# Optimization experiments

Hardware: AMD Instinct MI355X
Metric: run time of the kernel (lower is better)

Reference implementation:

```python
import jax, jax.numpy as jnp
import numpy as np
import math

D_MODEL = 1024
NUM_HEADS = 16
D_K = D_MODEL // NUM_HEADS
B, S = 2, 2048


def setup_inputs() -> dict:
    key = jax.random.key(0)
    ks = jax.random.split(key, 13)
    scale = 1.0 / math.sqrt(D_MODEL)
    inp = {
        "q": jax.random.normal(ks[0], (B, S, D_MODEL), jnp.float32),
        "k": jax.random.normal(ks[1], (B, S, D_MODEL), jnp.float32),
        "v": jax.random.normal(ks[2], (B, S, D_MODEL), jnp.float32),
        "mask": jax.random.randint(ks[3], (B, 1, S, S), 0, 2, jnp.int32),
        # torch nn.Linear params: y = x @ W.T + b
        "wQ_w": jax.random.normal(ks[4], (D_MODEL, D_MODEL), jnp.float32) * scale,
        "wQ_b": jax.random.normal(ks[5], (D_MODEL,), jnp.float32) * scale,
        "wK_w": jax.random.normal(ks[6], (D_MODEL, D_MODEL), jnp.float32) * scale,
        "wK_b": jax.random.normal(ks[7], (D_MODEL,), jnp.float32) * scale,
        "wV_w": jax.random.normal(ks[8], (D_MODEL, D_MODEL), jnp.float32) * scale,
        "wV_b": jax.random.normal(ks[9], (D_MODEL,), jnp.float32) * scale,
        "wO_w": jax.random.normal(ks[10], (D_MODEL, D_MODEL), jnp.float32) * scale,
        "wO_b": jax.random.normal(ks[11], (D_MODEL,), jnp.float32) * scale,
    }
    return inp


def _split_heads(x):
    # [B, S, D] -> [B, H, S, dK]
    b, s, _ = x.shape
    return x.reshape(b, s, NUM_HEADS, D_K).transpose(0, 2, 1, 3)


def reference(q, k, v, mask, wQ_w, wQ_b, wK_w, wK_b, wV_w, wV_b, wO_w, wO_b):
    qh = _split_heads(q @ wQ_w.T + wQ_b)
    kh = _split_heads(k @ wK_w.T + wK_b)
    vh = _split_heads(v @ wV_w.T + wV_b)
    # scores: [B, H, S, S] -- materialized as in the original module
    scores = jnp.einsum("bhsd,bhtd->bhst", qh, kh) / math.sqrt(D_K)
    scores = jnp.where(mask == 0, jnp.float32(-1e9), scores)
    attn = jax.nn.softmax(scores, axis=-1)
    out = jnp.einsum("bhst,bhtd->bhsd", attn, vh)  # [B, H, S, dK]
    out = out.transpose(0, 2, 1, 3).reshape(q.shape[0], -1, D_MODEL)
    return out @ wO_w.T + wO_b
```

## Files before the change

kernel.cpp:

```cpp
#include <hip/hip_runtime.h>
#include <hip/hip_bf16.h>
#include <stdint.h>
#include <math.h>

#define NHEADS 16
#define DK 64
#define BATCH 2
#define SEQ 2048
#define DMODEL 1024
#define MROWS (BATCH*SEQ)

typedef __bf16 bf16x8 __attribute__((ext_vector_type(8)));
typedef float  f32x4  __attribute__((ext_vector_type(4)));
typedef float  f32x16 __attribute__((ext_vector_type(16)));

typedef const __attribute__((address_space(1))) void* gas_ptr;
typedef       __attribute__((address_space(3))) void* las_ptr;

__device__ __forceinline__ void async16(const void* g, void* l) {
  __builtin_amdgcn_global_load_lds((gas_ptr)g, (las_ptr)l, 16, 0, 0);
}

__device__ __forceinline__ unsigned short f2bf_raw(float f) {
  __hip_bfloat16 h = __float2bfloat16(f);
  return *reinterpret_cast<unsigned short*>(&h);
}

__device__ __forceinline__ float fast_exp2(float x) {
#if __has_builtin(__builtin_amdgcn_exp2f)
  return __builtin_amdgcn_exp2f(x);
#else
  float r;
  asm("v_exp_f32 %0, %1\ns_nop 1" : "=v"(r) : "v"(x));
  return r;
#endif
}

__device__ __forceinline__ uint32_t pk_bf16(float lo, float hi2) {
  uint32_t r;
  asm("v_cvt_pk_bf16_f32 %0, %1, %2" : "=v"(r) : "v"(lo), "v"(hi2));
  return r;
}

__device__ __forceinline__ void half_swap(uint32_t& a, uint32_t& b) {
  auto r = __builtin_amdgcn_permlane32_swap(a, b, false, false);
  a = (uint32_t)r[0];
  b = (uint32_t)r[1];
}

__device__ __forceinline__ float mask_sel(uint32_t msel, float s, float c) {
  uint32_t su = __float_as_uint(s), cu = __float_as_uint(c);
  return __uint_as_float((msel & su) | (~msel & cu));
}

__device__ __forceinline__ f32x16 zero16() {
  f32x16 z;
#pragma unroll
  for (int i = 0; i < 16; ++i) z[i] = 0.f;
  return z;
}

__global__ void prep_kernel(const float* __restrict__ q,
                            const float* __restrict__ k,
                            const float* __restrict__ v,
                            const float* __restrict__ w0,
                            const float* __restrict__ w1,
                            const float* __restrict__ w2,
                            const float* __restrict__ w3,
                            ushort4* __restrict__ out,
                            const int* __restrict__ mask,
                            uint32_t* __restrict__ bits) {
  if (blockIdx.x < 16384) {
    int i = blockIdx.x * 256 + threadIdx.x;
    const float* src;
    int local;
    if (i < 3145728) {
      int seg = i >> 20;
      src = (seg == 0) ? q : (seg == 1) ? k : v;
      local = i & 1048575;
    } else {
      int j = i - 3145728;
      int seg = j >> 18;
      src = (seg == 0) ? w0 : (seg == 1) ? w1 : (seg == 2) ? w2 : w3;
      local = j & 262143;
    }
    float4 f = reinterpret_cast<const float4*>(src)[local];
    ushort4 u;
    u.x = f2bf_raw(f.x); u.y = f2bf_raw(f.y);
    u.z = f2bf_raw(f.z); u.w = f2bf_raw(f.w);
    out[i] = u;
  } else {
    int bi = blockIdx.x - 16384;
    int lane = threadIdx.x & 63, wid = threadIdx.x >> 6;
    size_t base = (size_t)bi * 1024 + (size_t)wid * 256;
    int4 q4 = reinterpret_cast<const int4*>(mask + base)[lane];
    uint32_t nib = (q4.x != 0 ? 1u : 0u) | (q4.y != 0 ? 2u : 0u) |
                   (q4.z != 0 ? 4u : 0u) | (q4.w != 0 ? 8u : 0u);
    nib <<= (lane & 7) * 4;
    nib |= (uint32_t)__shfl_xor((int)nib, 1);
    nib |= (uint32_t)__shfl_xor((int)nib, 2);
    nib |= (uint32_t)__shfl_xor((int)nib, 4);
    if ((lane & 7) == 0) bits[(base >> 5) + (lane >> 3)] = nib;
  }
}


__device__ __forceinline__ void gemm_core_128(
    const __hip_bfloat16* __restrict__ A, const __hip_bfloat16* __restrict__ Bw,
    int K, int m0, int n0,
    __hip_bfloat16* sA, __hip_bfloat16* sB, f32x4 acc[4][4]) {
  const int lane = threadIdx.x & 63;
  const int wid  = threadIdx.x >> 6;
  const int wr = wid >> 1, wc = wid & 1;
  const int l15 = lane & 15, lg = lane >> 4;
  const int sw = l15 & 7;
  const int crow8 = lane >> 3;
  const int cslot = lane & 7;

#pragma unroll
  for (int mi = 0; mi < 4; ++mi)
#pragma unroll
    for (int ni = 0; ni < 4; ++ni) acc[mi][ni] = f32x4{0.f, 0.f, 0.f, 0.f};

  for (int k0 = 0; k0 < K; k0 += 64) {
#pragma unroll
    for (int c0 = 0; c0 < 4; ++c0) {
      int c = wid + c0 * 4;
      int row = c * 8 + crow8;
      int scol = (cslot ^ (row & 7)) * 8;
      async16(A  + (size_t)(m0 + row) * K + k0 + scol,
              (char*)sA + c * 1024 + lane * 16);
      async16(Bw + (size_t)(n0 + row) * K + k0 + scol,
              (char*)sB + c * 1024 + lane * 16);
    }
    __syncthreads();
#pragma unroll
    for (int kc = 0; kc < 2; ++kc) {
      bf16x8 af[4], bfr[4];
#pragma unroll
      for (int mi = 0; mi < 4; ++mi)
        af[mi] = *reinterpret_cast<const bf16x8*>(
            &sA[(wr * 64 + mi * 16 + l15) * 64 + (((kc * 4 + lg) ^ sw) * 8)]);
#pragma unroll
      for (int ni = 0; ni < 4; ++ni)
        bfr[ni] = *reinterpret_cast<const bf16x8*>(
            &sB[(wc * 64 + ni * 16 + l15) * 64 + (((kc * 4 + lg) ^ sw) * 8)]);
      __builtin_amdgcn_s_setprio(1);
#pragma unroll
      for (int mi = 0; mi < 4; ++mi)
#pragma unroll
        for (int ni = 0; ni < 4; ++ni)
          acc[mi][ni] = __builtin_amdgcn_mfma_f32_16x16x32_bf16(
              af[mi], bfr[ni], acc[mi][ni], 0, 0, 0);
      __builtin_amdgcn_s_setprio(0);
    }
    __syncthreads();
  }
}

__global__ __launch_bounds__(256, 3) void qkv_gemm_kernel(
    const __hip_bfloat16* __restrict__ Xq, const __hip_bfloat16* __restrict__ Xk,
    const __hip_bfloat16* __restrict__ Xv,
    const __hip_bfloat16* __restrict__ Wq, const __hip_bfloat16* __restrict__ Wk,
    const __hip_bfloat16* __restrict__ Wv,
    const float* __restrict__ bq, const float* __restrict__ bk,
    const float* __restrict__ bv,
    __hip_bfloat16* __restrict__ Qh, __hip_bfloat16* __restrict__ Kh,
    __hip_bfloat16* __restrict__ VhT) {
  __shared__ __attribute__((aligned(16))) char smem[128 * 136 * 2];
  __hip_bfloat16* sA = (__hip_bfloat16*)smem;
  __hip_bfloat16* sB = (__hip_bfloat16*)(smem + 16384);
  const int z = blockIdx.z;
  const __hip_bfloat16* A  = (z == 0) ? Xq : (z == 1) ? Xk : Xv;
  const __hip_bfloat16* Bw = (z == 0) ? Wq : (z == 1) ? Wk : Wv;
  const float* bias        = (z == 0) ? bq : (z == 1) ? bk : bv;
  __hip_bfloat16* Co       = (z == 0) ? Qh : (z == 1) ? Kh : VhT;
  const int m0 = blockIdx.x * 128, n0 = blockIdx.y * 128;
  f32x4 acc[4][4];
  gemm_core_128(A, Bw, DMODEL, m0, n0, sA, sB, acc);

  const int tid = threadIdx.x, lane = tid & 63, wid = tid >> 6;
  const int wr = wid >> 1, wc = wid & 1;
  const int l15 = lane & 15, lg = lane >> 4;
  const float osc = (z == 0) ? 0.18033688f : 1.0f;
  const int PITCH = 136;
  __hip_bfloat16* sT = (__hip_bfloat16*)smem;

  if (z != 2) {
#pragma unroll
    for (int mi = 0; mi < 4; ++mi)
#pragma unroll
      for (int ni = 0; ni < 4; ++ni) {
        int jl = wc * 64 + ni * 16 + l15;
        float bj = bias[n0 + jl];
#pragma unroll
        for (int r = 0; r < 4; ++r) {
          int il = wr * 64 + mi * 16 + lg * 4 + r;
          sT[il * PITCH + jl] = __float2bfloat16((acc[mi][ni][r] + bj) * osc);
        }
      }
    __syncthreads();
#pragma unroll
    for (int u = 0; u < 8; ++u) {
      int t2 = tid + u * 256;
      int row = t2 >> 4, c8 = (t2 & 15) * 8;
      bf16x8 val = *reinterpret_cast<const bf16x8*>(&sT[row * PITCH + c8]);
      int ig = m0 + row, jg = n0 + c8;
      int bb = ig >> 11, s = ig & 2047, hh = jg >> 6, d = jg & 63;
      *reinterpret_cast<bf16x8*>(
          &Co[((size_t)(bb * NHEADS + hh) * SEQ + s) * DK + d]) = val;
    }
  } else {
#pragma unroll
    for (int mi = 0; mi < 4; ++mi)
#pragma unroll
      for (int ni = 0; ni < 4; ++ni) {
        int jl = wc * 64 + ni * 16 + l15;
        float bj = bias[n0 + jl];
        int il0 = wr * 64 + mi * 16 + lg * 4;
        ushort4 st4;
        st4.x = f2bf_raw(acc[mi][ni][0] + bj);
        st4.y = f2bf_raw(acc[mi][ni][1] + bj);
        st4.z = f2bf_raw(acc[mi][ni][2] + bj);
        st4.w = f2bf_raw(acc[mi][ni][3] + bj);
        *reinterpret_cast<ushort4*>(&sT[jl * PITCH + il0]) = st4;
      }
    __syncthreads();
#pragma unroll
    for (int u = 0; u < 8; ++u) {
      int t2 = tid + u * 256;
      int row = t2 >> 4, i8 = (t2 & 15) * 8;
      bf16x8 val = *reinterpret_cast<const bf16x8*>(&sT[row * PITCH + i8]);
      int jg = n0 + row, hh = jg >> 6, d = jg & 63;
      int ig0 = m0 + i8, bb = ig0 >> 11, s0 = ig0 & 2047;
      *reinterpret_cast<bf16x8*>(
          &Co[((size_t)(bb * NHEADS + hh) * DK + d) * SEQ + s0]) = val;
    }
  }
}

__global__ __launch_bounds__(256, 3) void out_gemm_kernel(
    const __hip_bfloat16* __restrict__ A, const __hip_bfloat16* __restrict__ Ww,
    const float* __restrict__ bias, float* __restrict__ C) {
  __shared__ __attribute__((aligned(16))) char smem[32768];
  __hip_bfloat16* sA = (__hip_bfloat16*)smem;
  __hip_bfloat16* sB = (__hip_bfloat16*)(smem + 16384);
  const int m0 = blockIdx.x * 128, n0 = blockIdx.y * 128;
  f32x4 acc[4][4];
  gemm_core_128(A, Ww, DMODEL, m0, n0, sA, sB, acc);
  const int lane = threadIdx.x & 63, wid = threadIdx.x >> 6;
  const int wr = wid >> 1, wc = wid & 1;
#pragma unroll
  for (int mi = 0; mi < 4; ++mi)
#pragma unroll
    for (int ni = 0; ni < 4; ++ni) {
      int j = n0 + wc * 64 + ni * 16 + (lane & 15);
      float bj = bias[j];
#pragma unroll
      for (int r = 0; r < 4; ++r) {
        int i = m0 + wr * 64 + mi * 16 + (lane >> 4) * 4 + r;
        C[(size_t)i * DMODEL + j] = acc[mi][ni][r] + bj;
      }
    }
}


__global__ __launch_bounds__(512, 4) void attn_kernel(
    const __hip_bfloat16* __restrict__ Qh, const __hip_bfloat16* __restrict__ Kh,
    const __hip_bfloat16* __restrict__ VhT, const uint32_t* __restrict__ mbits,
    __hip_bfloat16* __restrict__ AO) {
  __shared__ char pool[65536 + 512 + 512];
  __hip_bfloat16* Kpool = (__hip_bfloat16*)pool;
  __hip_bfloat16* Vpool = (__hip_bfloat16*)(pool + 32768);
  float* sRed = (float*)(pool + 65536);
  float* lC   = (float*)(pool + 65536 + 512);
  float* accC = (float*)pool;

  const int tid = threadIdx.x, lane = tid & 63, wid = tid >> 6;
  const int grp = wid >> 2, wq = wid & 3;
  const int ltid = tid & 255;
  const int l31 = lane & 31, hi = lane >> 5;
  const int sw = l31 & 7;
  const int bh = blockIdx.y, b = bh >> 4, h = bh & 15;
  const int q0g = blockIdx.x * 128 + wq * 32;
  const int kvbase = grp * (SEQ / 2);

  const __hip_bfloat16* Qp = Qh  + (size_t)bh * SEQ * DK;
  const __hip_bfloat16* Kp = Kh  + (size_t)bh * SEQ * DK;
  const __hip_bfloat16* Vp = VhT + (size_t)bh * DK * SEQ;
  const uint32_t* mb = mbits + (size_t)b * SEQ * (SEQ / 32)
                             + (size_t)(q0g + l31) * (SEQ / 32) + (kvbase >> 5);
  float* sRedW = &sRed[wq * 32];

  bf16x8 qf[4];
#pragma unroll
  for (int dc = 0; dc < 4; ++dc)
    qf[dc] = *reinterpret_cast<const bf16x8*>(
        &Qp[(size_t)(q0g + l31) * DK + dc * 16 + hi * 8]);

  f32x16 acc0 = zero16(), acc1 = zero16();
  float l_run = 0.f;

#define STAGE(kv0_, s_)                                                        \
  {                                                                            \
    _Pragma("unroll")                                                          \
    for (int u = 0; u < 2; ++u) {                                              \
      int c = ltid + u * 256;                                                  \
      int row = c >> 3, ss = (c & 7) ^ (row & 7);                              \
      async16(Kp + (size_t)(kvbase + (kv0_) + row) * DK + ss * 8,              \
              (char*)(Kpool + (grp * 2 + (s_)) * 4096) + c * 16);              \
      async16(Vp + (size_t)row * SEQ + kvbase + (kv0_) + ss * 8,               \
              (char*)(Vpool + (grp * 2 + (s_)) * 4096) + c * 16);              \
    }                                                                          \
  }

  STAGE(0, 0);
  uint2 mw = *reinterpret_cast<const uint2*>(mb);
  asm volatile("s_waitcnt vmcnt(0)" ::: "memory");
  __syncthreads();

  const int NT = SEQ / 2 / 64;
  for (int t = 0; t < NT; ++t) {
    const int cur = t & 1;
    if (t + 1 < NT) STAGE((t + 1) * 64, cur ^ 1);

    uint2 mw_next;
    if (t + 1 < NT) mw_next = *reinterpret_cast<const uint2*>(mb + (t + 1) * 2);
    uint32_t w0 = mw.x >> (4 * hi), w1 = mw.y >> (4 * hi);

    const __hip_bfloat16* ks = Kpool + (grp * 2 + cur) * 4096;
    const __hip_bfloat16* vs = Vpool + (grp * 2 + cur) * 4096;

    f32x16 s0 = zero16(), s1 = zero16();
    __builtin_amdgcn_s_setprio(1);
#pragma unroll
    for (int dc = 0; dc < 4; ++dc) {
      bf16x8 k0 = *reinterpret_cast<const bf16x8*>(
          &ks[(size_t)(l31) * 64 + (((dc * 2 + hi) ^ sw) * 8)]);
      bf16x8 k1 = *reinterpret_cast<const bf16x8*>(
          &ks[(size_t)(32 + l31) * 64 + (((dc * 2 + hi) ^ sw) * 8)]);
      s0 = __builtin_amdgcn_mfma_f32_32x32x16_bf16(k0, qf[dc], s0, 0, 0, 0);
      s1 = __builtin_amdgcn_mfma_f32_32x32x16_bf16(k1, qf[dc], s1, 0, 0, 0);
    }
    __builtin_amdgcn_s_setprio(0);

    union { uint32_t u[4]; bf16x8 v; } pc;
    {
      float p[16];
#pragma unroll
      for (int r = 0; r < 16; ++r) {
        const int sh = (r & 3) + 8 * (r >> 2);
        uint32_t msel = (uint32_t)__builtin_amdgcn_sbfe((int)w0, sh, 1);
        p[r] = fast_exp2(mask_sel(msel, s0[r], -1e9f));
        l_run += p[r];
      }
      uint32_t a0 = pk_bf16(p[0], p[1]),  a1 = pk_bf16(p[2], p[3]);
      uint32_t b0 = pk_bf16(p[4], p[5]),  b1 = pk_bf16(p[6], p[7]);
      uint32_t c0 = pk_bf16(p[8], p[9]),  c1 = pk_bf16(p[10], p[11]);
      uint32_t d0 = pk_bf16(p[12], p[13]), d1 = pk_bf16(p[14], p[15]);
      half_swap(a0, b0); half_swap(a1, b1);
      half_swap(c0, d0); half_swap(c1, d1);
      __builtin_amdgcn_s_setprio(1);
      pc.u[0] = a0; pc.u[1] = a1; pc.u[2] = b0; pc.u[3] = b1;
      {
        bf16x8 v0 = *reinterpret_cast<const bf16x8*>(
            &vs[(size_t)(l31) * 64 + (((0 + hi) ^ sw) * 8)]);
        bf16x8 v1 = *reinterpret_cast<const bf16x8*>(
            &vs[(size_t)(32 + l31) * 64 + (((0 + hi) ^ sw) * 8)]);
        acc0 = __builtin_amdgcn_mfma_f32_32x32x16_bf16(pc.v, v0, acc0, 0, 0, 0);
        acc1 = __builtin_amdgcn_mfma_f32_32x32x16_bf16(pc.v, v1, acc1, 0, 0, 0);
      }
      pc.u[0] = c0; pc.u[1] = c1; pc.u[2] = d0; pc.u[3] = d1;
      {
        bf16x8 v0 = *reinterpret_cast<const bf16x8*>(
            &vs[(size_t)(l31) * 64 + (((2 + hi) ^ sw) * 8)]);
        bf16x8 v1 = *reinterpret_cast<const bf16x8*>(
            &vs[(size_t)(32 + l31) * 64 + (((2 + hi) ^ sw) * 8)]);
        acc0 = __builtin_amdgcn_mfma_f32_32x32x16_bf16(pc.v, v0, acc0, 0, 0, 0);
        acc1 = __builtin_amdgcn_mfma_f32_32x32x16_bf16(pc.v, v1, acc1, 0, 0, 0);
      }
      __builtin_amdgcn_s_setprio(0);
    }
    {
      float p[16];
#pragma unroll
      for (int r = 0; r < 16; ++r) {
        const int sh = (r & 3) + 8 * (r >> 2);
        uint32_t msel = (uint32_t)__builtin_amdgcn_sbfe((int)w1, sh, 1);
        p[r] = fast_exp2(mask_sel(msel, s1[r], -1e9f));
        l_run += p[r];
      }
      uint32_t a0 = pk_bf16(p[0], p[1]),  a1 = pk_bf16(p[2], p[3]);
      uint32_t b0 = pk_bf16(p[4], p[5]),  b1 = pk_bf16(p[6], p[7]);
      uint32_t c0 = pk_bf16(p[8], p[9]),  c1 = pk_bf16(p[10], p[11]);
      uint32_t d0 = pk_bf16(p[12], p[13]), d1 = pk_bf16(p[14], p[15]);
      half_swap(a0, b0); half_swap(a1, b1);
      half_swap(c0, d0); half_swap(c1, d1);
      __builtin_amdgcn_s_setprio(1);
      pc.u[0] = a0; pc.u[1] = a1; pc.u[2] = b0; pc.u[3] = b1;
      {
        bf16x8 v0 = *reinterpret_cast<const bf16x8*>(
            &vs[(size_t)(l31) * 64 + (((4 + hi) ^ sw) * 8)]);
        bf16x8 v1 = *reinterpret_cast<const bf16x8*>(
            &vs[(size_t)(32 + l31) * 64 + (((4 + hi) ^ sw) * 8)]);
        acc0 = __builtin_amdgcn_mfma_f32_32x32x16_bf16(pc.v, v0, acc0, 0, 0, 0);
        acc1 = __builtin_amdgcn_mfma_f32_32x32x16_bf16(pc.v, v1, acc1, 0, 0, 0);
      }
      pc.u[0] = c0; pc.u[1] = c1; pc.u[2] = d0; pc.u[3] = d1;
      {
        bf16x8 v0 = *reinterpret_cast<const bf16x8*>(
            &vs[(size_t)(l31) * 64 + (((6 + hi) ^ sw) * 8)]);
        bf16x8 v1 = *reinterpret_cast<const bf16x8*>(
            &vs[(size_t)(32 + l31) * 64 + (((6 + hi) ^ sw) * 8)]);
        acc0 = __builtin_amdgcn_mfma_f32_32x32x16_bf16(pc.v, v0, acc0, 0, 0, 0);
        acc1 = __builtin_amdgcn_mfma_f32_32x32x16_bf16(pc.v, v1, acc1, 0, 0, 0);
      }
      __builtin_amdgcn_s_setprio(0);
    }

    mw = mw_next;
    asm volatile("s_waitcnt vmcnt(0)" ::: "memory");
    __syncthreads();
  }

  l_run += __shfl_xor(l_run, 32);

  if (grp == 1) {
    float* myacc = &accC[(wq * 64 + lane) * 32];
#pragma unroll
    for (int r = 0; r < 16; ++r) { myacc[r] = acc0[r]; myacc[16 + r] = acc1[r]; }
    if (hi == 0) lC[wq * 32 + l31] = l_run;
  }
  __syncthreads();

  if (grp == 0) {
    const float* oacc = &accC[(wq * 64 + lane) * 32];
#pragma unroll
    for (int r = 0; r < 16; ++r) { acc0[r] += oacc[r]; acc1[r] += oacc[16 + r]; }
    float l_tot = l_run + lC[wq * 32 + l31];
    if (hi == 0) sRedW[l31] = l_tot;
    asm volatile("s_waitcnt lgkmcnt(0)" ::: "memory");
#pragma unroll
    for (int r = 0; r < 16; ++r) {
      int cr = (r & 3) + 8 * (r >> 2) + 4 * hi;
      float linv = 1.0f / sRedW[cr];
      int qrow = q0g + cr;
      size_t base = ((size_t)b * SEQ + qrow) * DMODEL + h * 64 + l31;
      AO[base]      = __float2bfloat16(acc0[r] * linv);
      AO[base + 32] = __float2bfloat16(acc1[r] * linv);
    }
  }
}


extern "C" void kernel_launch(void* const* d_in, const int* in_sizes, int n_in,
                              void* d_out, int out_size, void* d_ws, size_t ws_size,
                              hipStream_t stream) {
  const float* q    = (const float*)d_in[0];
  const float* k    = (const float*)d_in[1];
  const float* v    = (const float*)d_in[2];
  const int*   mask = (const int*)d_in[3];
  const float* wQ_w = (const float*)d_in[4];
  const float* wQ_b = (const float*)d_in[5];
  const float* wK_w = (const float*)d_in[6];
  const float* wK_b = (const float*)d_in[7];
  const float* wV_w = (const float*)d_in[8];
  const float* wV_b = (const float*)d_in[9];
  const float* wO_w = (const float*)d_in[10];
  const float* wO_b = (const float*)d_in[11];

  char* ws = (char*)d_ws;
  const size_t SZ_X = (size_t)MROWS * DMODEL * 2;
  const size_t SZ_W = (size_t)DMODEL * DMODEL * 2;
  __hip_bfloat16* Xq  = (__hip_bfloat16*)(ws);
  __hip_bfloat16* Xk  = (__hip_bfloat16*)(ws + SZ_X);
  __hip_bfloat16* Xv  = (__hip_bfloat16*)(ws + 2 * SZ_X);
  __hip_bfloat16* Wq  = (__hip_bfloat16*)(ws + 3 * SZ_X);
  __hip_bfloat16* Wk  = (__hip_bfloat16*)(ws + 3 * SZ_X + SZ_W);
  __hip_bfloat16* Wv  = (__hip_bfloat16*)(ws + 3 * SZ_X + 2 * SZ_W);
  __hip_bfloat16* Wo  = (__hip_bfloat16*)(ws + 3 * SZ_X + 3 * SZ_W);
  __hip_bfloat16* Qh  = (__hip_bfloat16*)(ws + 3 * SZ_X + 4 * SZ_W);
  __hip_bfloat16* Kh  = (__hip_bfloat16*)(ws + 4 * SZ_X + 4 * SZ_W);
  __hip_bfloat16* VhT = (__hip_bfloat16*)(ws + 5 * SZ_X + 4 * SZ_W);
  __hip_bfloat16* AO  = (__hip_bfloat16*)(ws + 6 * SZ_X + 4 * SZ_W);
  uint32_t*       MB  = (uint32_t*)      (ws + 7 * SZ_X + 4 * SZ_W);

  prep_kernel<<<24576, 256, 0, stream>>>(q, k, v, wQ_w, wK_w, wV_w, wO_w,
                                         (ushort4*)ws, mask, MB);

  qkv_gemm_kernel<<<dim3(MROWS / 128, DMODEL / 128, 3), 256, 0, stream>>>(
      Xq, Xk, Xv, Wq, Wk, Wv, wQ_b, wK_b, wV_b, Qh, Kh, VhT);

  attn_kernel<<<dim3(SEQ / 128, BATCH * NHEADS), 512, 0, stream>>>(
      Qh, Kh, VhT, MB, AO);

  out_gemm_kernel<<<dim3(MROWS / 128, DMODEL / 128), 256, 0, stream>>>(
      AO, Wo, wO_b, (float*)d_out);
}
```

Baseline: 237.8 us.

## Split prep kernel, halve out-GEMM tile rows, launch attention per batch

Splits the combined cast/mask prep kernel into two separate kernels. Rewrites the output GEMM to use 64x128 tiles with a single-stage LDS load per k-step, which doubles the grid to fill more CUs. Splits the attention launch into two per-batch launches via a head offset. These changes aim to improve occupancy and load balance, at the cost of extra launch overhead and a GEMM loop that no longer overlaps loads with compute.

```diff
diff --git a/kernel.cpp b/kernel.cpp
--- a/kernel.cpp
+++ b/kernel.cpp
@@ -60,48 +60,47 @@
   return z;
 }
 
-__global__ void prep_kernel(const float* __restrict__ q,
+__global__ void cast_kernel(const float* __restrict__ q,
                             const float* __restrict__ k,
                             const float* __restrict__ v,
                             const float* __restrict__ w0,
                             const float* __restrict__ w1,
                             const float* __restrict__ w2,
                             const float* __restrict__ w3,
-                            ushort4* __restrict__ out,
-                            const int* __restrict__ mask,
+                            ushort4* __restrict__ out) {
+  int i = blockIdx.x * 256 + threadIdx.x;
+  const float* src;
+  int local;
+  if (i < 3145728) {
+    int seg = i >> 20;
+    src = (seg == 0) ? q : (seg == 1) ? k : v;
+    local = i & 1048575;
+  } else {
+    int j = i - 3145728;
+    int seg = j >> 18;
+    src = (seg == 0) ? w0 : (seg == 1) ? w1 : (seg == 2) ? w2 : w3;
+    local = j & 262143;
+  }
+  float4 f = reinterpret_cast<const float4*>(src)[local];
+  ushort4 u;
+  u.x = f2bf_raw(f.x); u.y = f2bf_raw(f.y);
+  u.z = f2bf_raw(f.z); u.w = f2bf_raw(f.w);
+  out[i] = u;
+}
+
+__global__ void mask_kernel(const int* __restrict__ mask,
                             uint32_t* __restrict__ bits) {
-  if (blockIdx.x < 16384) {
-    int i = blockIdx.x * 256 + threadIdx.x;
-    const float* src;
-    int local;
-    if (i < 3145728) {
-      int seg = i >> 20;
-      src = (seg == 0) ? q : (seg == 1) ? k : v;
-      local = i & 1048575;
-    } else {
-      int j = i - 3145728;
-      int seg = j >> 18;
-      src = (seg == 0) ? w0 : (seg == 1) ? w1 : (seg == 2) ? w2 : w3;
-      local = j & 262143;
-    }
-    float4 f = reinterpret_cast<const float4*>(src)[local];
-    ushort4 u;
-    u.x = f2bf_raw(f.x); u.y = f2bf_raw(f.y);
-    u.z = f2bf_raw(f.z); u.w = f2bf_raw(f.w);
-    out[i] = u;
-  } else {
-    int bi = blockIdx.x - 16384;
-    int lane = threadIdx.x & 63, wid = threadIdx.x >> 6;
-    size_t base = (size_t)bi * 1024 + (size_t)wid * 256;
-    int4 q4 = reinterpret_cast<const int4*>(mask + base)[lane];
-    uint32_t nib = (q4.x != 0 ? 1u : 0u) | (q4.y != 0 ? 2u : 0u) |
-                   (q4.z != 0 ? 4u : 0u) | (q4.w != 0 ? 8u : 0u);
-    nib <<= (lane & 7) * 4;
-    nib |= (uint32_t)__shfl_xor((int)nib, 1);
-    nib |= (uint32_t)__shfl_xor((int)nib, 2);
-    nib |= (uint32_t)__shfl_xor((int)nib, 4);
-    if ((lane & 7) == 0) bits[(base >> 5) + (lane >> 3)] = nib;
-  }
+  int bi = blockIdx.x;
+  int lane = threadIdx.x & 63, wid = threadIdx.x >> 6;
+  size_t base = (size_t)bi * 1024 + (size_t)wid * 256;
+  int4 q4 = reinterpret_cast<const int4*>(mask + base)[lane];
+  uint32_t nib = (q4.x != 0 ? 1u : 0u) | (q4.y != 0 ? 2u : 0u) |
+                 (q4.z != 0 ? 4u : 0u) | (q4.w != 0 ? 8u : 0u);
+  nib <<= (lane & 7) * 4;
+  nib |= (uint32_t)__shfl_xor((int)nib, 1);
+  nib |= (uint32_t)__shfl_xor((int)nib, 2);
+  nib |= (uint32_t)__shfl_xor((int)nib, 4);
+  if ((lane & 7) == 0) bits[(base >> 5) + (lane >> 3)] = nib;
 }
 
 
@@ -242,23 +241,73 @@
 __global__ __launch_bounds__(256, 3) void out_gemm_kernel(
     const __hip_bfloat16* __restrict__ A, const __hip_bfloat16* __restrict__ Ww,
     const float* __restrict__ bias, float* __restrict__ C) {
-  __shared__ __attribute__((aligned(16))) char smem[32768];
+  __shared__ __attribute__((aligned(16))) char smem[8192 + 16384];
   __hip_bfloat16* sA = (__hip_bfloat16*)smem;
-  __hip_bfloat16* sB = (__hip_bfloat16*)(smem + 16384);
-  const int m0 = blockIdx.x * 128, n0 = blockIdx.y * 128;
-  f32x4 acc[4][4];
-  gemm_core_128(A, Ww, DMODEL, m0, n0, sA, sB, acc);
+  __hip_bfloat16* sB = (__hip_bfloat16*)(smem + 8192);
+  const int m0 = blockIdx.x * 64, n0 = blockIdx.y * 128;
   const int lane = threadIdx.x & 63, wid = threadIdx.x >> 6;
   const int wr = wid >> 1, wc = wid & 1;
-#pragma unroll
-  for (int mi = 0; mi < 4; ++mi)
+  const int l15 = lane & 15, lg = lane >> 4;
+  const int sw = l15 & 7;
+  const int crow8 = lane >> 3;
+  const int cslot = lane & 7;
+
+  f32x4 acc[2][4];
+#pragma unroll
+  for (int mi = 0; mi < 2; ++mi)
+#pragma unroll
+    for (int ni = 0; ni < 4; ++ni) acc[mi][ni] = f32x4{0.f, 0.f, 0.f, 0.f};
+
+  for (int k0 = 0; k0 < DMODEL; k0 += 64) {
+#pragma unroll
+    for (int c0 = 0; c0 < 2; ++c0) {
+      int c = wid + c0 * 4;
+      int row = c * 8 + crow8;
+      int scol = (cslot ^ (row & 7)) * 8;
+      async16(A + (size_t)(m0 + row) * DMODEL + k0 + scol,
+              (char*)sA + c * 1024 + lane * 16);
+    }
+#pragma unroll
+    for (int c0 = 0; c0 < 4; ++c0) {
+      int c = wid + c0 * 4;
+      int row = c * 8 + crow8;
+      int scol = (cslot ^ (row & 7)) * 8;
+      async16(Ww + (size_t)(n0 + row) * DMODEL + k0 + scol,
+              (char*)sB + c * 1024 + lane * 16);
+    }
+    __syncthreads();
+#pragma unroll
+    for (int kc = 0; kc < 2; ++kc) {
+      bf16x8 af[2], bfr[4];
+#pragma unroll
+      for (int mi = 0; mi < 2; ++mi)
+        af[mi] = *reinterpret_cast<const bf16x8*>(
+            &sA[(wr * 32 + mi * 16 + l15) * 64 + (((kc * 4 + lg) ^ sw) * 8)]);
+#pragma unroll
+      for (int ni = 0; ni < 4; ++ni)
+        bfr[ni] = *reinterpret_cast<const bf16x8*>(
+            &sB[(wc * 64 + ni * 16 + l15) * 64 + (((kc * 4 + lg) ^ sw) * 8)]);
+      __builtin_amdgcn_s_setprio(1);
+#pragma unroll
+      for (int mi = 0; mi < 2; ++mi)
+#pragma unroll
+        for (int ni = 0; ni < 4; ++ni)
+          acc[mi][ni] = __builtin_amdgcn_mfma_f32_16x16x32_bf16(
+              af[mi], bfr[ni], acc[mi][ni], 0, 0, 0);
+      __builtin_amdgcn_s_setprio(0);
+    }
+    __syncthreads();
+  }
+
+#pragma unroll
+  for (int mi = 0; mi < 2; ++mi)
 #pragma unroll
     for (int ni = 0; ni < 4; ++ni) {
-      int j = n0 + wc * 64 + ni * 16 + (lane & 15);
+      int j = n0 + wc * 64 + ni * 16 + l15;
       float bj = bias[j];
 #pragma unroll
       for (int r = 0; r < 4; ++r) {
-        int i = m0 + wr * 64 + mi * 16 + (lane >> 4) * 4 + r;
+        int i = m0 + wr * 32 + mi * 16 + lg * 4 + r;
         C[(size_t)i * DMODEL + j] = acc[mi][ni][r] + bj;
       }
     }
@@ -268,7 +317,7 @@
 __global__ __launch_bounds__(512, 4) void attn_kernel(
     const __hip_bfloat16* __restrict__ Qh, const __hip_bfloat16* __restrict__ Kh,
     const __hip_bfloat16* __restrict__ VhT, const uint32_t* __restrict__ mbits,
-    __hip_bfloat16* __restrict__ AO) {
+    __hip_bfloat16* __restrict__ AO, int bh0) {
   __shared__ char pool[65536 + 512 + 512];
   __hip_bfloat16* Kpool = (__hip_bfloat16*)pool;
   __hip_bfloat16* Vpool = (__hip_bfloat16*)(pool + 32768);
@@ -281,7 +330,7 @@
   const int ltid = tid & 255;
   const int l31 = lane & 31, hi = lane >> 5;
   const int sw = l31 & 7;
-  const int bh = blockIdx.y, b = bh >> 4, h = bh & 15;
+  const int bh = bh0 + blockIdx.y, b = bh >> 4, h = bh & 15;
   const int q0g = blockIdx.x * 128 + wq * 32;
   const int kvbase = grp * (SEQ / 2);
 
@@ -485,15 +534,18 @@
   __hip_bfloat16* AO  = (__hip_bfloat16*)(ws + 6 * SZ_X + 4 * SZ_W);
   uint32_t*       MB  = (uint32_t*)      (ws + 7 * SZ_X + 4 * SZ_W);
 
-  prep_kernel<<<24576, 256, 0, stream>>>(q, k, v, wQ_w, wK_w, wV_w, wO_w,
-                                         (ushort4*)ws, mask, MB);
+  cast_kernel<<<16384, 256, 0, stream>>>(q, k, v, wQ_w, wK_w, wV_w, wO_w,
+                                         (ushort4*)ws);
+  mask_kernel<<<8192, 256, 0, stream>>>(mask, MB);
 
   qkv_gemm_kernel<<<dim3(MROWS / 128, DMODEL / 128, 3), 256, 0, stream>>>(
       Xq, Xk, Xv, Wq, Wk, Wv, wQ_b, wK_b, wV_b, Qh, Kh, VhT);
 
-  attn_kernel<<<dim3(SEQ / 128, BATCH * NHEADS), 512, 0, stream>>>(
-      Qh, Kh, VhT, MB, AO);
-
-  out_gemm_kernel<<<dim3(MROWS / 128, DMODEL / 128), 256, 0, stream>>>(
+  attn_kernel<<<dim3(SEQ / 128, NHEADS), 512, 0, stream>>>(
+      Qh, Kh, VhT, MB, AO, 0);
+  attn_kernel<<<dim3(SEQ / 128, NHEADS), 512, 0, stream>>>(
+      Qh, Kh, VhT, MB, AO, NHEADS);
+
+  out_gemm_kernel<<<dim3(MROWS / 64, DMODEL / 128), 256, 0, stream>>>(
       AO, Wo, wO_b, (float*)d_out);
 }
```

After: 257.3 us. +8.2%, slower.
